# Kernel tuning notes

Measured on AMD Instinct MI355X. Metric: run time of the kernel, lower is better.

## Reference

```python
import jax, jax.numpy as jnp
import numpy as np

B = 4096          # fused tokens (batch)
E = 1024          # attnConfig embed_size == MoE emb_size
OUT = E // 4      # per-branch feature dim (self.output)
N_EXP = 8         # number of experts
TOP = 2           # top-k routing
H = 8             # attention heads
HD = E // H       # head dim
HID = 4 * E       # expert MLP hidden
IMG = 64 * 64     # flattened single-channel image
W_IMP = 0.01      # importance loss weight


def setup_inputs() -> dict:
    key = jax.random.key(0)
    ks = jax.random.split(key, 24)
    n = lambda i, shp, sc=1.0: jax.random.normal(ks[i], shp, jnp.float32) * sc
    inp = {
        'source': n(0, (B, 1, 64, 64)),
        'target': n(1, (B, 1, 64, 64)),
        'background': n(2, (B, 1, 64, 64)),
        'image': n(3, (B, E)),
        'text': n(4, (B, E)),
        # shared encoder (stub: flatten -> fc to OUT, shared across s/t/b)
        'W_enc': n(5, (IMG, OUT), 0.02), 'b_enc': jnp.zeros((OUT,), jnp.float32),
        # linerImg
        'W_img': n(6, (E, OUT), 0.02), 'b_img': jnp.zeros((OUT,), jnp.float32),
        # cross attention
        'Wq': n(7, (E, E), 0.02), 'bq': jnp.zeros((E,), jnp.float32),
        'Wk': n(8, (E, E), 0.02), 'bk': jnp.zeros((E,), jnp.float32),
        'Wv': n(9, (E, E), 0.02), 'bv': jnp.zeros((E,), jnp.float32),
        'Wo': n(10, (E, E), 0.02), 'bo': jnp.zeros((E,), jnp.float32),
        # gate
        'W_gate': n(11, (E, N_EXP), 0.02), 'b_gate': jnp.zeros((N_EXP,), jnp.float32),
        # experts: per-expert 2-layer MLP E->HID->E
        'W1': n(12, (N_EXP, E, HID), 0.02), 'b1': jnp.zeros((N_EXP, HID), jnp.float32),
        'W2': n(13, (N_EXP, HID, E), 0.02), 'b2': jnp.zeros((N_EXP, E), jnp.float32),
    }
    return inp


def reference(source, target, background, image, text,
              W_enc, b_enc, W_img, b_img,
              Wq, bq, Wk, bk, Wv, bv, Wo, bo,
              W_gate, b_gate, W1, b1, W2, b2):
    enc = lambda a: a.reshape(a.shape[0], -1) @ W_enc + b_enc      # shared_encoder stub
    s = enc(source); t = enc(target); bg = enc(background)        # [B, OUT] each
    img = jax.nn.silu(image @ W_img + b_img)                      # [B, OUT]
    x = jnp.concatenate([s, t, bg, img], axis=1)                  # [B, E] visionFeatures

    # cross attention with seq_len 1 for both x (query) and text (key/value)
    q = (x @ Wq + bq).reshape(B, H, HD)
    k = (text @ Wk + bk).reshape(B, H, HD)
    v = (text @ Wv + bv).reshape(B, H, HD)
    scores = jnp.sum(q * k, axis=-1, keepdims=True) / jnp.sqrt(jnp.float32(HD))  # [B,H,1]
    attw = jax.nn.softmax(scores[..., None], axis=-1)[..., 0]     # softmax over 1 key == 1
    att = (attw * v).reshape(B, E) @ Wo + bo                       # [B, E]

    gate_logits = att @ W_gate + b_gate                            # [B, N_EXP]
    gate_prob = jax.nn.softmax(gate_logits, axis=-1)               # eval mode: no noise
    top_w, top_idx = jax.lax.top_k(gate_prob, TOP)                 # [B, TOP]
    top_w = jax.nn.softmax(top_w, axis=-1)                         # renormalize over top-k

    # dense-dispatch equivalent of the per-expert gather/index_add loop
    h = jax.nn.gelu(jnp.einsum('be,neh->nbh', x, W1) + b1[:, None, :])   # [N,B,HID]
    y_all = jnp.einsum('nbh,nhe->nbe', h, W2) + b2[:, None, :]           # [N,B,E]
    combine = jnp.zeros((B, N_EXP), jnp.float32).at[
        jnp.arange(B)[:, None], top_idx].add(top_w)                      # [B,N]
    y = jnp.einsum('nbe,bn->be', y_all, combine)                          # [B,E]

    importance = gate_prob.sum(axis=0)                             # [N_EXP]
    importance_loss = W_IMP * (jnp.std(importance, ddof=1) / jnp.mean(importance)) ** 2
    return (y, gate_prob, importance_loss)
```

## Files before the change

### kernel.cpp

```cpp
#include <hip/hip_runtime.h>
#include <hip/hip_bf16.h>
#include <stdint.h>

typedef __bf16 bf16_t;
typedef bf16_t bf16x8 __attribute__((ext_vector_type(8)));
typedef float f32x4 __attribute__((ext_vector_type(4)));
typedef uint16_t u16x8 __attribute__((ext_vector_type(8)));

static constexpr int B_TOK  = 4096;
static constexpr int E_DIM  = 1024;
static constexpr int N_EXPC = 8;
static constexpr int HID    = 4096;
static constexpr int IMGSZ  = 4096;
static constexpr int NSLOT  = 2 * B_TOK;
static constexpr int NTIL   = 71;

#define DEVI __device__ __forceinline__

DEVI int imin(int a, int b) { return a < b ? a : b; }

DEVI uint16_t f2bf(float f) {
  union { float f; uint32_t u; } v; v.f = f;
  uint32_t u = v.u;
  return (uint16_t)((u + 0x7FFFu + ((u >> 16) & 1u)) >> 16);
}

DEVI void gload_lds16(const void* g, void* l) {
  __builtin_amdgcn_global_load_lds((const __attribute__((address_space(1))) void*)g,
                                   (__attribute__((address_space(3))) void*)l, 16, 0, 0);
}

template<int N> DEVI void waitv() {
  if constexpr (N == 0)       asm volatile("s_waitcnt vmcnt(0)" ::: "memory");
  else if constexpr (N == 3)  asm volatile("s_waitcnt vmcnt(3)" ::: "memory");
  else if constexpr (N == 4)  asm volatile("s_waitcnt vmcnt(4)" ::: "memory");
  else if constexpr (N == 10) asm volatile("s_waitcnt vmcnt(10)" ::: "memory");
}

#define BAR() do { __builtin_amdgcn_sched_barrier(0); __builtin_amdgcn_s_barrier(); \
                   __builtin_amdgcn_sched_barrier(0); } while (0)

#define MFMA16(a, b, c) __builtin_amdgcn_mfma_f32_16x16x32_bf16((a), (b), (c), 0, 0, 0)

__global__ __launch_bounds__(256)
void transW(const float* __restrict__ W1, const float* __restrict__ W2,
            const float* __restrict__ We, const float* __restrict__ Wi,
            uint16_t* __restrict__ W1T, uint16_t* __restrict__ W2T,
            uint16_t* __restrict__ WeT, uint16_t* __restrict__ WiT)
{
  __shared__ float tile[64][65];
  int bid = blockIdx.x;
  const float* in; uint16_t* out; int R, C, c0, r0;
  if (bid < 8192) {
    int e = bid >> 10, rem = bid & 1023;
    R = 1024; C = 4096;
    c0 = (rem & 63) * 64; r0 = (rem >> 6) * 64;
    in = W1 + (size_t)e * R * C; out = W1T + (size_t)e * R * C;
  } else if (bid < 16384) {
    int i = bid - 8192; int e = i >> 10, rem = i & 1023;
    R = 4096; C = 1024;
    c0 = (rem & 15) * 64; r0 = (rem >> 4) * 64;
    in = W2 + (size_t)e * R * C; out = W2T + (size_t)e * R * C;
  } else if (bid < 16640) {
    int i = bid - 16384;
    R = 4096; C = 256;
    c0 = (i & 3) * 64; r0 = (i >> 2) * 64;
    in = We; out = WeT;
  } else {
    int i = bid - 16640;
    R = 1024; C = 256;
    c0 = (i & 3) * 64; r0 = (i >> 2) * 64;
    in = Wi; out = WiT;
  }
  int t = threadIdx.x;
  #pragma unroll
  for (int i = 0; i < 4; ++i) {
    int rr = i * 16 + (t >> 4), c4 = (t & 15) * 4;
    f32x4 v = *(const f32x4*)&in[(size_t)(r0 + rr) * C + c0 + c4];
    tile[rr][c4 + 0] = v[0]; tile[rr][c4 + 1] = v[1];
    tile[rr][c4 + 2] = v[2]; tile[rr][c4 + 3] = v[3];
  }
  __syncthreads();
  #pragma unroll
  for (int i = 0; i < 2; ++i) {
    int c = i * 32 + (t >> 3), j = t & 7;
    u16x8 o;
    #pragma unroll
    for (int k = 0; k < 8; ++k) o[k] = f2bf(tile[j * 8 + k][c]);
    *(u16x8*)&out[(size_t)(c0 + c) * R + r0 + j * 8] = o;
  }
}

template<int BN, int EPI, bool GATHER, int NT, int KSPLIT>
__global__ __launch_bounds__(256, 5)
void gemm_p(const uint16_t* __restrict__ Ab, int lda,
            const uint16_t* __restrict__ BT, void* __restrict__ Cv, int ldc,
            const float* __restrict__ bias, int K,
            const int* __restrict__ meta, const int* __restrict__ perm,
            size_t bStride, int biasStride, size_t cPlane)
{
  constexpr int HN = BN / 2, FN = BN / 32;
  constexpr int OPS = (BN == 128 ? 4 : 3);
  constexpr int NT2 = NT * KSPLIT;
  constexpr int TOTAL = NTIL * NT2, Q = TOTAL / 8, FULLB = 64 * NT2;
  int bid = blockIdx.x;
  int wg = (bid & 7) * Q + (bid >> 3);
  int mtile, nt2;
  if (wg < FULLB) { int rem = wg % (8 * NT2); mtile = (wg / (8 * NT2)) * 8 + (rem & 7); nt2 = rem >> 3; }
  else            { int rem = wg - FULLB;     mtile = 64 + rem % 7;                     nt2 = rem / 7; }
  if (mtile >= meta[0]) return;
  int nt = nt2 % NT, kc = nt2 / NT;
  int e = meta[1 + 3 * mtile], rowBase = meta[2 + 3 * mtile], rows = meta[3 + 3 * mtile];
  int Kc = K / KSPLIT, k0 = kc * Kc;
  const uint16_t* Bt = BT + (size_t)e * bStride;
  const float* bi = bias + (size_t)e * (size_t)biasStride;

  constexpr int ABUF = 8192;
  constexpr int BBUF = (BN == 128) ? 8192 : 4096;
  __shared__ __align__(16) char sAraw[2 * ABUF];
  __shared__ __align__(16) char sBraw[2 * BBUF];

  int t = threadIdx.x, wave = t >> 6, lane = t & 63;
  int wr = wave >> 1, wc = wave & 1;

  int rB = t >> 2;
  int slB = ((t & 3) ^ (rB & 3)) * 8;
  const uint16_t* gB0 = Bt + (size_t)(nt * BN + rB) * K + k0 + slB;
  const uint16_t* gB1 = Bt + (size_t)(nt * BN + rB + 64) * K + k0 + slB;

  int r0 = t >> 2, r1 = r0 + 64;
  int sl = ((t & 3) ^ (r0 & 3)) * 8;
  int rr0 = imin(r0, rows - 1), rr1 = imin(r1, rows - 1);
  int car0 = GATHER ? perm[rowBase + rr0] : rowBase + rr0;
  int car1 = GATHER ? perm[rowBase + rr1] : rowBase + rr1;
  const uint16_t* gA0 = Ab + (size_t)car0 * lda + k0 + sl;
  const uint16_t* gA1 = Ab + (size_t)car1 * lda + k0 + sl;

  char* laW = sAraw + wave * 1024;
  char* lbW = sBraw + wave * 1024;
  auto STAGE = [&](int kt, int c) {
    int ko = kt << 5;
    char* la = laW + c * ABUF;
    char* lb = lbW + c * BBUF;
    gload_lds16(gA0 + ko, la);
    gload_lds16(gA1 + ko, la + 4096);
    gload_lds16(gB0 + ko, lb);
    if constexpr (BN == 128) gload_lds16(gB1 + ko, lb + 4096);
  };

  f32x4 acc[4][FN];
  #pragma unroll
  for (int m = 0; m < 4; m++)
    #pragma unroll
    for (int n = 0; n < FN; n++)
      acc[m][n] = f32x4{0.f, 0.f, 0.f, 0.f};

  STAGE(0, 0);

  int fr = lane & 15;
  int rdoff = ((lane >> 4) ^ (lane & 3)) * 16;
  int nk = Kc >> 5;

  for (int kt = 0; kt < nk; ++kt) {
    int b = kt & 1, nb = b ^ 1;
    bool more = kt + 1 < nk;
    if (more) { STAGE(kt + 1, nb); waitv<OPS>(); }
    else waitv<0>();
    BAR();

    const char* bA = sAraw + b * ABUF;
    const char* bB = sBraw + b * BBUF;
    bf16x8 af[4], bfr[FN];
    #pragma unroll
    for (int m = 0; m < 4; m++)
      af[m] = *(const bf16x8*)(bA + (wr * 64 + m * 16 + fr) * 64 + rdoff);
    #pragma unroll
    for (int n = 0; n < FN; n++)
      bfr[n] = *(const bf16x8*)(bB + (wc * HN + n * 16 + fr) * 64 + rdoff);
    #pragma unroll
    for (int m = 0; m < 4; m++)
      #pragma unroll
      for (int n = 0; n < FN; n++)
        acc[m][n] = MFMA16(af[m], bfr[n], acc[m][n]);

    BAR();
  }

  #pragma unroll
  for (int m = 0; m < 4; m++) {
    int lrow = wr * 64 + m * 16 + (lane >> 4) * 4;
    #pragma unroll
    for (int n = 0; n < FN; n++) {
      int col = nt * BN + wc * HN + n * 16 + (lane & 15);
      float bval = (EPI == 3) ? bi[col] : 0.f;
      #pragma unroll
      for (int r = 0; r < 4; r++) {
        int lr = lrow + r;
        if (lr >= rows) continue;
        float v = acc[m][n][r] + bval;
        size_t cr = (size_t)kc * cPlane + (size_t)(rowBase + lr) * ldc + col;
        if (EPI == 3) {
          float u = v + 0.044715f * v * v * v;
          v = v / (1.f + __expf(-1.5957691216057308f * u));
          ((uint16_t*)Cv)[cr] = f2bf(v);
        } else {
          ((float*)Cv)[cr] = v;
        }
      }
    }
  }
}

template<int SPLITK>
__global__ __launch_bounds__(256, 3)
void gemm_encR(const float* __restrict__ F0, const float* __restrict__ F1,
               const float* __restrict__ F2, int lda,
               const uint16_t* __restrict__ BT, float* __restrict__ P, int K)
{
  int z = blockIdx.z, br = z / SPLITK, kc = z % SPLITK;
  const float* Af = (br == 0) ? F0 : (br == 1) ? F1 : F2;
  int Kc = K / SPLITK, k0 = kc * Kc;
  int rowBase = blockIdx.x * 64, nt = blockIdx.y;

  __shared__ __align__(16) char sB[3 * 8192];
  int t = threadIdx.x, wave = t >> 6, lane = t & 63;
  int fr = lane & 15, q4 = lane >> 4;

  const float* gA = Af + (size_t)(rowBase + wave * 16 + fr) * lda + k0 + q4 * 8;

  int rloc = t >> 2;
  int ssw = ((t & 3) ^ (rloc & 3)) * 8;
  const uint16_t* gB0 = BT + (size_t)(nt * 128 + rloc) * K + k0 + ssw;
  const uint16_t* gB1 = gB0 + (size_t)64 * K;

  auto STB = [&](int kt, int c) {
    gload_lds16(gB0 + kt * 32, sB + c * 8192 + wave * 1024);
    gload_lds16(gB1 + kt * 32, sB + c * 8192 + 4096 + wave * 1024);
  };

  f32x4 acc[8];
  #pragma unroll
  for (int n = 0; n < 8; ++n) acc[n] = f32x4{0.f, 0.f, 0.f, 0.f};

  int nk = Kc >> 5;
  STB(0, 0); STB(1, 1);
  f32x4 aE0 = *(const f32x4*)(gA),      aE1 = *(const f32x4*)(gA + 4);
  f32x4 aO0 = *(const f32x4*)(gA + 32), aO1 = *(const f32x4*)(gA + 36);
  int c0 = 0, c2 = 2;
  int bRow = (q4 ^ (fr & 3)) * 16;

  auto step = [&](int kt, f32x4& aX0, f32x4& aX1) {
    bool m2 = kt + 2 < nk;
    if (m2) STB(kt + 2, c2);
    bf16x8 a;
    a[0] = (bf16_t)aX0[0]; a[1] = (bf16_t)aX0[1]; a[2] = (bf16_t)aX0[2]; a[3] = (bf16_t)aX0[3];
    a[4] = (bf16_t)aX1[0]; a[5] = (bf16_t)aX1[1]; a[6] = (bf16_t)aX1[2]; a[7] = (bf16_t)aX1[3];
    int kp = m2 ? kt + 2 : kt;
    aX0 = *(const f32x4*)(gA + kp * 32);
    aX1 = *(const f32x4*)(gA + kp * 32 + 4);
    if (m2) waitv<10>(); else waitv<0>();
    BAR();
    const char* bb = sB + c0 * 8192;
    bf16x8 bfr[8];
    #pragma unroll
    for (int n = 0; n < 8; ++n)
      bfr[n] = *(const bf16x8*)(bb + n * 1024 + fr * 64 + bRow);
    #pragma unroll
    for (int n = 0; n < 8; ++n) acc[n] = MFMA16(a, bfr[n], acc[n]);
    BAR();
    c0 = (c0 == 2) ? 0 : c0 + 1;
    c2 = (c2 == 2) ? 0 : c2 + 1;
  };

  for (int kt = 0; kt < nk; kt += 2) {
    step(kt, aE0, aE1);
    step(kt + 1, aO0, aO1);
  }

  #pragma unroll
  for (int n = 0; n < 8; ++n) {
    int col = nt * 128 + n * 16 + fr;
    #pragma unroll
    for (int r = 0; r < 4; ++r) {
      int row = rowBase + wave * 16 + q4 * 4 + r;
      P[((size_t)z * B_TOK + row) * 256 + col] = acc[n][r];
    }
  }
}

template<int SK, bool SILU>
__global__ __launch_bounds__(256)
void redu_k(const float* __restrict__ P, const float* __restrict__ bias,
            uint16_t* __restrict__ xb, int colBase)
{
  int br = blockIdx.y;
  int row = blockIdx.x * 4 + (threadIdx.x >> 6);
  int c4 = (threadIdx.x & 63) * 4;
  f32x4 s = *(const f32x4*)&bias[c4];
  const float* p = P + ((size_t)br * SK * B_TOK + row) * 256 + c4;
  #pragma unroll
  for (int kc = 0; kc < SK; ++kc)
    s += *(const f32x4*)(p + (size_t)kc * B_TOK * 256);
  if (SILU) {
    #pragma unroll
    for (int j = 0; j < 4; ++j) s[j] = s[j] / (1.f + __expf(-s[j]));
  }
  ushort4 o;
  o.x = f2bf(s[0]); o.y = f2bf(s[1]); o.z = f2bf(s[2]); o.w = f2bf(s[3]);
  *(ushort4*)&xb[(size_t)row * E_DIM + colBase + br * 256 + c4] = o;
}

__global__ __launch_bounds__(256)
void bvwo_k(const float* __restrict__ bv, const float* __restrict__ Wo,
            float* __restrict__ part)
{
  int b = blockIdx.x, t = threadIdx.x;
  f32x4 acc = {0.f, 0.f, 0.f, 0.f};
  for (int k = b * 128; k < b * 128 + 128; ++k) {
    float s = bv[k];
    f32x4 w = *(const f32x4*)&Wo[(size_t)k * E_DIM + t * 4];
    acc[0] = __builtin_fmaf(s, w[0], acc[0]);
    acc[1] = __builtin_fmaf(s, w[1], acc[1]);
    acc[2] = __builtin_fmaf(s, w[2], acc[2]);
    acc[3] = __builtin_fmaf(s, w[3], acc[3]);
  }
  *(f32x4*)&part[(size_t)b * E_DIM + t * 4] = acc;
}

__global__ void t1red_k(const float* __restrict__ part, const float* __restrict__ bo,
                        float* __restrict__ t1)
{
  int j = blockIdx.x * 256 + threadIdx.x;
  float s = bo[j];
  for (int b = 0; b < 8; ++b) s += part[(size_t)b * E_DIM + j];
  t1[j] = s;
}

__global__ __launch_bounds__(256)
void matf_k(const float* __restrict__ W, const float* __restrict__ G,
            float* __restrict__ out)
{
  int k = blockIdx.x * 4 + (threadIdx.x >> 6);
  int lane = threadIdx.x & 63;
  float a0 = 0.f, a1 = 0.f, a2 = 0.f, a3 = 0.f, a4 = 0.f, a5 = 0.f, a6 = 0.f, a7 = 0.f;
  for (int m = lane; m < E_DIM; m += 64) {
    float w = W[(size_t)k * E_DIM + m];
    const float* gm = &G[m * 8];
    a0 = __builtin_fmaf(w, gm[0], a0); a1 = __builtin_fmaf(w, gm[1], a1);
    a2 = __builtin_fmaf(w, gm[2], a2); a3 = __builtin_fmaf(w, gm[3], a3);
    a4 = __builtin_fmaf(w, gm[4], a4); a5 = __builtin_fmaf(w, gm[5], a5);
    a6 = __builtin_fmaf(w, gm[6], a6); a7 = __builtin_fmaf(w, gm[7], a7);
  }
  #pragma unroll
  for (int off = 32; off; off >>= 1) {
    a0 += __shfl_xor(a0, off); a1 += __shfl_xor(a1, off);
    a2 += __shfl_xor(a2, off); a3 += __shfl_xor(a3, off);
    a4 += __shfl_xor(a4, off); a5 += __shfl_xor(a5, off);
    a6 += __shfl_xor(a6, off); a7 += __shfl_xor(a7, off);
  }
  if (lane == 0) {
    float* o = &out[k * 8];
    o[0] = a0; o[1] = a1; o[2] = a2; o[3] = a3;
    o[4] = a4; o[5] = a5; o[6] = a6; o[7] = a7;
  }
}

__global__ __launch_bounds__(512)
void gbias_k(const float* __restrict__ t1, const float* __restrict__ Wg,
             const float* __restrict__ bg, float* __restrict__ gb)
{
  int e = threadIdx.x >> 6, lane = threadIdx.x & 63;
  float s = 0.f;
  for (int m = lane; m < E_DIM; m += 64) s = __builtin_fmaf(t1[m], Wg[m * 8 + e], s);
  #pragma unroll
  for (int off = 32; off; off >>= 1) s += __shfl_xor(s, off);
  if (lane == 0) gb[e] = s + bg[e];
}

__global__ __launch_bounds__(256)
void gate_k(const float* __restrict__ text, const float* __restrict__ G3,
            const float* __restrict__ gb, float* __restrict__ gate_out,
            int* __restrict__ topIdx, float* __restrict__ topW,
            int* __restrict__ counts)
{
  __shared__ __align__(16) float sT[E_DIM];
  __shared__ float lg[8];
  int b = blockIdx.x, t = threadIdx.x;
  *(f32x4*)&sT[t * 4] = *(const f32x4*)&text[(size_t)b * E_DIM + t * 4];
  __syncthreads();
  int wave = t >> 6, lane = t & 63;
  #pragma unroll
  for (int ei = 0; ei < 2; ++ei) {
    int e = wave * 2 + ei;
    float s = 0.f;
    for (int k = lane; k < E_DIM; k += 64) s = __builtin_fmaf(sT[k], G3[k * 8 + e], s);
    #pragma unroll
    for (int off = 32; off; off >>= 1) s += __shfl_down(s, off);
    if (lane == 0) lg[e] = s + gb[e];
  }
  __syncthreads();
  if (t == 0) {
    float p[8];
    float mx = lg[0];
    for (int i = 1; i < 8; i++) mx = fmaxf(mx, lg[i]);
    float den = 0.f;
    for (int i = 0; i < 8; i++) { p[i] = __expf(lg[i] - mx); den += p[i]; }
    float inv = 1.f / den;
    for (int i = 0; i < 8; i++) { p[i] *= inv; gate_out[(size_t)b * 8 + i] = p[i]; }
    int i1 = 0;
    for (int i = 1; i < 8; i++) if (p[i] > p[i1]) i1 = i;
    int i2 = (i1 == 0) ? 1 : 0;
    for (int i = 0; i < 8; i++) if (i != i1 && p[i] > p[i2]) i2 = i;
    float ex = __expf(p[i2] - p[i1]);
    float w1 = 1.f / (1.f + ex), w2 = ex / (1.f + ex);
    topIdx[b * 2] = i1; topIdx[b * 2 + 1] = i2;
    topW[b * 2] = w1;  topW[b * 2 + 1] = w2;
    atomicAdd(&counts[i1], 1);
    atomicAdd(&counts[i2], 1);
  }
}

__global__ void imp_k(const float* __restrict__ gate_out, float* __restrict__ imp)
{
  int e = blockIdx.x, t = threadIdx.x;
  float s = 0.f;
  for (int b = t; b < B_TOK; b += 256) s += gate_out[(size_t)b * 8 + e];
  __shared__ float red[256];
  red[t] = s; __syncthreads();
  for (int off = 128; off; off >>= 1) { if (t < off) red[t] += red[t + off]; __syncthreads(); }
  if (t == 0) imp[e] = red[0];
}

__global__ void loss_k(const float* __restrict__ imp, float* __restrict__ out_loss)
{
  if (threadIdx.x == 0 && blockIdx.x == 0) {
    float m = 0.f;
    for (int e = 0; e < 8; e++) m += imp[e];
    m *= 0.125f;
    float v = 0.f;
    for (int e = 0; e < 8; e++) { float d = imp[e] - m; v += d * d; }
    v /= 7.f;
    out_loss[0] = 0.01f * v / (m * m);
  }
}

__global__ void zero_k(int* counts, int* cursor)
{
  int t = threadIdx.x;
  if (t < 8) { counts[t] = 0; cursor[t] = 0; }
}

__global__ void scan_k(const int* __restrict__ counts, int* __restrict__ bases,
                       int* __restrict__ meta)
{
  if (threadIdx.x == 0) {
    int a = 0, nt = 0;
    for (int e = 0; e < 8; e++) {
      bases[e] = a;
      int c = counts[e];
      for (int j = 0; j < c; j += 128) {
        meta[1 + 3 * nt] = e;
        meta[2 + 3 * nt] = a + j;
        meta[3 + 3 * nt] = (c - j < 128) ? (c - j) : 128;
        nt++;
      }
      a += c;
    }
    meta[0] = nt;
  }
}

__global__ void fill_k(const int* __restrict__ topIdx, int* __restrict__ cursor,
                       const int* __restrict__ bases, int* __restrict__ perm,
                       int* __restrict__ slotOf)
{
  int b = blockIdx.x * 256 + threadIdx.x;
  if (b < B_TOK) {
    #pragma unroll
    for (int j = 0; j < 2; j++) {
      int e = topIdx[b * 2 + j];
      int pos = atomicAdd(&cursor[e], 1);
      int slot = bases[e] + pos;
      perm[slot] = b;
      slotOf[b * 2 + j] = slot;
    }
  }
}

__global__ __launch_bounds__(256)
void combine_k(const float* __restrict__ Yp, const int* __restrict__ slotOf,
               const int* __restrict__ topIdx, const float* __restrict__ topW,
               const float* __restrict__ b2, float* __restrict__ y)
{
  int b = blockIdx.x, t = threadIdx.x;
  int s0 = slotOf[b * 2], s1 = slotOf[b * 2 + 1];
  int e0 = topIdx[b * 2], e1 = topIdx[b * 2 + 1];
  float w0 = topW[b * 2], w1 = topW[b * 2 + 1];
  int c = t * 4;
  size_t P1 = (size_t)NSLOT * E_DIM;
  f32x4 x0 = *(const f32x4*)&Yp[(size_t)s0 * E_DIM + c];
  x0 += *(const f32x4*)&Yp[P1 + (size_t)s0 * E_DIM + c];
  x0 += *(const f32x4*)&b2[(size_t)e0 * E_DIM + c];
  f32x4 x1 = *(const f32x4*)&Yp[(size_t)s1 * E_DIM + c];
  x1 += *(const f32x4*)&Yp[P1 + (size_t)s1 * E_DIM + c];
  x1 += *(const f32x4*)&b2[(size_t)e1 * E_DIM + c];
  f32x4 r = x0 * w0 + x1 * w1;
  *(f32x4*)&y[(size_t)b * E_DIM + c] = r;
}

extern "C" void kernel_launch(void* const* d_in, const int* in_sizes, int n_in,
                              void* d_out, int out_size, void* d_ws, size_t ws_size,
                              hipStream_t stream)
{
  (void)in_sizes; (void)n_in; (void)out_size;
  const float* src   = (const float*)d_in[0];
  const float* tgt   = (const float*)d_in[1];
  const float* bgr   = (const float*)d_in[2];
  const float* image = (const float*)d_in[3];
  const float* text  = (const float*)d_in[4];
  const float* W_enc = (const float*)d_in[5];
  const float* b_enc = (const float*)d_in[6];
  const float* W_img = (const float*)d_in[7];
  const float* b_img = (const float*)d_in[8];
  const float* Wv    = (const float*)d_in[13];
  const float* bv    = (const float*)d_in[14];
  const float* Wo    = (const float*)d_in[15];
  const float* bo    = (const float*)d_in[16];
  const float* Wg    = (const float*)d_in[17];
  const float* bgg   = (const float*)d_in[18];
  const float* W1    = (const float*)d_in[19];
  const float* b1    = (const float*)d_in[20];
  const float* W2    = (const float*)d_in[21];
  const float* b2    = (const float*)d_in[22];

  float* out_y    = (float*)d_out;
  float* out_gate = out_y + (size_t)B_TOK * E_DIM;
  float* out_loss = out_gate + (size_t)B_TOK * N_EXPC;

  char* p = (char*)d_ws;
  auto alloc = [&](size_t bytes) { char* r = p; p += (bytes + 255) & ~(size_t)255; return r; };
  uint16_t* WencT = (uint16_t*)alloc((size_t)256 * IMGSZ * 2);
  uint16_t* WimgT = (uint16_t*)alloc((size_t)256 * E_DIM * 2);
  uint16_t* W1T   = (uint16_t*)alloc((size_t)N_EXPC * HID * E_DIM * 2);
  uint16_t* W2T   = (uint16_t*)alloc((size_t)N_EXPC * E_DIM * HID * 2);
  float* part  = (float*)alloc((size_t)8 * E_DIM * 4);
  float* g1c   = (float*)alloc((size_t)E_DIM * 8 * 4);
  float* G3    = (float*)alloc((size_t)E_DIM * 8 * 4);
  float* t1    = (float*)alloc(E_DIM * 4);
  float* gbv   = (float*)alloc(64 * 4);
  float* impb  = (float*)alloc(64 * 4);
  int*   topIdx = (int*)alloc(B_TOK * 2 * 4);
  float* topW   = (float*)alloc(B_TOK * 2 * 4);
  int*   slotOf = (int*)alloc(B_TOK * 2 * 4);
  int*   counts = (int*)alloc(64 * 4);
  int*   bases  = (int*)alloc(64 * 4);
  int*   cursor = (int*)alloc(64 * 4);
  int*   meta   = (int*)alloc((1 + 3 * (NTIL + 1)) * 4 + 64);
  int*   perm   = (int*)alloc(NSLOT * 4);
  uint16_t* xbf  = (uint16_t*)alloc((size_t)B_TOK * E_DIM * 2);
  uint16_t* Hbuf = (uint16_t*)alloc((size_t)NSLOT * HID * 2);
  char* uni = alloc((size_t)2 * NSLOT * E_DIM * 4);
  float* Penc = (float*)uni;
  float* Pimg = Penc + (size_t)12 * B_TOK * 256;
  float* Yp   = (float*)uni;
  if ((size_t)(p - (char*)d_ws) > ws_size) return;

  zero_k<<<1, 64, 0, stream>>>(counts, cursor);

  transW<<<dim3(16704), 256, 0, stream>>>(W1, W2, W_enc, W_img, W1T, W2T, WencT, WimgT);

  bvwo_k<<<8, 256, 0, stream>>>(bv, Wo, part);
  t1red_k<<<4, 256, 0, stream>>>(part, bo, t1);
  matf_k<<<256, 256, 0, stream>>>(Wo, Wg, g1c);
  matf_k<<<256, 256, 0, stream>>>(Wv, g1c, G3);
  gbias_k<<<1, 512, 0, stream>>>(t1, Wg, bgg, gbv);
  gate_k<<<B_TOK, 256, 0, stream>>>(text, G3, gbv, out_gate, topIdx, topW, counts);
  imp_k<<<8, 256, 0, stream>>>(out_gate, impb);
  loss_k<<<1, 64, 0, stream>>>(impb, out_loss);
  scan_k<<<1, 64, 0, stream>>>(counts, bases, meta);
  fill_k<<<16, 256, 0, stream>>>(topIdx, cursor, bases, perm, slotOf);

  gemm_encR<4><<<dim3(B_TOK / 64, 2, 12), 256, 0, stream>>>(
      src, tgt, bgr, IMGSZ, WencT, Penc, IMGSZ);
  gemm_encR<2><<<dim3(B_TOK / 64, 2, 2), 256, 0, stream>>>(
      image, image, image, E_DIM, WimgT, Pimg, E_DIM);
  redu_k<4, false><<<dim3(B_TOK / 4, 3), 256, 0, stream>>>(Penc, b_enc, xbf, 0);
  redu_k<2, true><<<dim3(B_TOK / 4, 1), 256, 0, stream>>>(Pimg, b_img, xbf, 768);

  gemm_p<128, 3, true, HID / 128, 1><<<dim3(NTIL * (HID / 128)), 256, 0, stream>>>(
      xbf, E_DIM, W1T, Hbuf, HID, b1, E_DIM, meta, perm, (size_t)HID * E_DIM, HID, 0);
  gemm_p<128, 0, false, E_DIM / 128, 2><<<dim3(NTIL * (E_DIM / 128) * 2), 256, 0, stream>>>(
      Hbuf, HID, W2T, Yp, E_DIM, b2, HID, meta, perm, (size_t)E_DIM * HID, E_DIM,
      (size_t)NSLOT * E_DIM);

  combine_k<<<B_TOK, 256, 0, stream>>>(Yp, slotOf, topIdx, topW, b2, out_y);
}
```

Before: 709.5 us.

## Fuse top-k combine into second expert GEMM epilogue via atomic scatter-add

The second expert GEMM now scales each output row by its routing weight and atomically adds it straight into the zeroed output, adding the bias in the epilogue. This removes the split-K partial buffer, the separate combine kernel and the large fp32 intermediate traffic. In exchange, split-K is dropped, which halves the number of workgroups, and float atomics add contention and make the summation order nondeterministic. Several small routing kernels are also merged (importance plus loss, scan plus fill using shared-memory cursors), and the output is zeroed with a memset.

```diff
diff --git a/kernel.cpp b/kernel.cpp
--- a/kernel.cpp
+++ b/kernel.cpp
@@ -97,6 +97,7 @@
             const uint16_t* __restrict__ BT, void* __restrict__ Cv, int ldc,
             const float* __restrict__ bias, int K,
             const int* __restrict__ meta, const int* __restrict__ perm,
+            const float* __restrict__ wSlot,
             size_t bStride, int biasStride, size_t cPlane)
 {
   constexpr int HN = BN / 2, FN = BN / 32;
@@ -186,25 +187,42 @@
     BAR();
   }
 
-  #pragma unroll
-  for (int m = 0; m < 4; m++) {
-    int lrow = wr * 64 + m * 16 + (lane >> 4) * 4;
-    #pragma unroll
-    for (int n = 0; n < FN; n++) {
-      int col = nt * BN + wc * HN + n * 16 + (lane & 15);
-      float bval = (EPI == 3) ? bi[col] : 0.f;
+  if constexpr (EPI == 4) {
+    float* outY = (float*)Cv;
+    #pragma unroll
+    for (int m = 0; m < 4; m++) {
       #pragma unroll
       for (int r = 0; r < 4; r++) {
-        int lr = lrow + r;
+        int lr = wr * 64 + m * 16 + (lane >> 4) * 4 + r;
         if (lr >= rows) continue;
-        float v = acc[m][n][r] + bval;
-        size_t cr = (size_t)kc * cPlane + (size_t)(rowBase + lr) * ldc + col;
-        if (EPI == 3) {
+        int slot = rowBase + lr;
+        int tok = perm[slot];
+        float w = wSlot[slot];
+        float* dst = outY + (size_t)tok * ldc;
+        #pragma unroll
+        for (int n = 0; n < FN; n++) {
+          int col = nt * BN + wc * HN + n * 16 + (lane & 15);
+          atomicAdd(dst + col, w * (acc[m][n][r] + bi[col]));
+        }
+      }
+    }
+  } else {
+    #pragma unroll
+    for (int m = 0; m < 4; m++) {
+      int lrow = wr * 64 + m * 16 + (lane >> 4) * 4;
+      #pragma unroll
+      for (int n = 0; n < FN; n++) {
+        int col = nt * BN + wc * HN + n * 16 + (lane & 15);
+        float bval = bi[col];
+        #pragma unroll
+        for (int r = 0; r < 4; r++) {
+          int lr = lrow + r;
+          if (lr >= rows) continue;
+          float v = acc[m][n][r] + bval;
+          size_t cr = (size_t)kc * cPlane + (size_t)(rowBase + lr) * ldc + col;
           float u = v + 0.044715f * v * v * v;
           v = v / (1.f + __expf(-1.5957691216057308f * u));
           ((uint16_t*)Cv)[cr] = f2bf(v);
-        } else {
-          ((float*)Cv)[cr] = v;
         }
       }
     }
@@ -420,43 +438,56 @@
   }
 }
 
-__global__ void imp_k(const float* __restrict__ gate_out, float* __restrict__ imp)
-{
-  int e = blockIdx.x, t = threadIdx.x;
-  float s = 0.f;
-  for (int b = t; b < B_TOK; b += 256) s += gate_out[(size_t)b * 8 + e];
-  __shared__ float red[256];
-  red[t] = s; __syncthreads();
-  for (int off = 128; off; off >>= 1) { if (t < off) red[t] += red[t + off]; __syncthreads(); }
-  if (t == 0) imp[e] = red[0];
-}
-
-__global__ void loss_k(const float* __restrict__ imp, float* __restrict__ out_loss)
-{
-  if (threadIdx.x == 0 && blockIdx.x == 0) {
+__global__ __launch_bounds__(256)
+void imploss_k(const float* __restrict__ gate_out, float* __restrict__ out_loss)
+{
+  int t = threadIdx.x;
+  float s[8] = {0.f, 0.f, 0.f, 0.f, 0.f, 0.f, 0.f, 0.f};
+  for (int b = t; b < B_TOK; b += 256) {
+    const float* g = &gate_out[(size_t)b * 8];
+    #pragma unroll
+    for (int e = 0; e < 8; ++e) s[e] += g[e];
+  }
+  __shared__ float red[8][256];
+  #pragma unroll
+  for (int e = 0; e < 8; ++e) red[e][t] = s[e];
+  __syncthreads();
+  for (int off = 128; off; off >>= 1) {
+    if (t < off)
+      #pragma unroll
+      for (int e = 0; e < 8; ++e) red[e][t] += red[e][t + off];
+    __syncthreads();
+  }
+  if (t == 0) {
     float m = 0.f;
-    for (int e = 0; e < 8; e++) m += imp[e];
+    for (int e = 0; e < 8; e++) m += red[e][0];
     m *= 0.125f;
     float v = 0.f;
-    for (int e = 0; e < 8; e++) { float d = imp[e] - m; v += d * d; }
+    for (int e = 0; e < 8; e++) { float d = red[e][0] - m; v += d * d; }
     v /= 7.f;
     out_loss[0] = 0.01f * v / (m * m);
   }
 }
 
-__global__ void zero_k(int* counts, int* cursor)
+__global__ void zero_k(int* counts)
 {
   int t = threadIdx.x;
-  if (t < 8) { counts[t] = 0; cursor[t] = 0; }
-}
-
-__global__ void scan_k(const int* __restrict__ counts, int* __restrict__ bases,
-                       int* __restrict__ meta)
-{
-  if (threadIdx.x == 0) {
+  if (t < 8) counts[t] = 0;
+}
+
+__global__ __launch_bounds__(256)
+void scanfill_k(const int* __restrict__ counts, const int* __restrict__ topIdx,
+                const float* __restrict__ topW,
+                int* __restrict__ meta, int* __restrict__ perm,
+                float* __restrict__ wSlot)
+{
+  __shared__ int sBases[8];
+  __shared__ int sCursor[8];
+  int t = threadIdx.x;
+  if (t == 0) {
     int a = 0, nt = 0;
     for (int e = 0; e < 8; e++) {
-      bases[e] = a;
+      sBases[e] = a; sCursor[e] = 0;
       int c = counts[e];
       for (int j = 0; j < c; j += 128) {
         meta[1 + 3 * nt] = e;
@@ -468,44 +499,17 @@
     }
     meta[0] = nt;
   }
-}
-
-__global__ void fill_k(const int* __restrict__ topIdx, int* __restrict__ cursor,
-                       const int* __restrict__ bases, int* __restrict__ perm,
-                       int* __restrict__ slotOf)
-{
-  int b = blockIdx.x * 256 + threadIdx.x;
-  if (b < B_TOK) {
+  __syncthreads();
+  for (int b = t; b < B_TOK; b += 256) {
     #pragma unroll
     for (int j = 0; j < 2; j++) {
       int e = topIdx[b * 2 + j];
-      int pos = atomicAdd(&cursor[e], 1);
-      int slot = bases[e] + pos;
+      int pos = atomicAdd(&sCursor[e], 1);
+      int slot = sBases[e] + pos;
       perm[slot] = b;
-      slotOf[b * 2 + j] = slot;
+      wSlot[slot] = topW[b * 2 + j];
     }
   }
-}
-
-__global__ __launch_bounds__(256)
-void combine_k(const float* __restrict__ Yp, const int* __restrict__ slotOf,
-               const int* __restrict__ topIdx, const float* __restrict__ topW,
-               const float* __restrict__ b2, float* __restrict__ y)
-{
-  int b = blockIdx.x, t = threadIdx.x;
-  int s0 = slotOf[b * 2], s1 = slotOf[b * 2 + 1];
-  int e0 = topIdx[b * 2], e1 = topIdx[b * 2 + 1];
-  float w0 = topW[b * 2], w1 = topW[b * 2 + 1];
-  int c = t * 4;
-  size_t P1 = (size_t)NSLOT * E_DIM;
-  f32x4 x0 = *(const f32x4*)&Yp[(size_t)s0 * E_DIM + c];
-  x0 += *(const f32x4*)&Yp[P1 + (size_t)s0 * E_DIM + c];
-  x0 += *(const f32x4*)&b2[(size_t)e0 * E_DIM + c];
-  f32x4 x1 = *(const f32x4*)&Yp[(size_t)s1 * E_DIM + c];
-  x1 += *(const f32x4*)&Yp[P1 + (size_t)s1 * E_DIM + c];
-  x1 += *(const f32x4*)&b2[(size_t)e1 * E_DIM + c];
-  f32x4 r = x0 * w0 + x1 * w1;
-  *(f32x4*)&y[(size_t)b * E_DIM + c] = r;
 }
 
 extern "C" void kernel_launch(void* const* d_in, const int* in_sizes, int n_in,
@@ -548,24 +552,21 @@
   float* G3    = (float*)alloc((size_t)E_DIM * 8 * 4);
   float* t1    = (float*)alloc(E_DIM * 4);
   float* gbv   = (float*)alloc(64 * 4);
-  float* impb  = (float*)alloc(64 * 4);
   int*   topIdx = (int*)alloc(B_TOK * 2 * 4);
   float* topW   = (float*)alloc(B_TOK * 2 * 4);
-  int*   slotOf = (int*)alloc(B_TOK * 2 * 4);
   int*   counts = (int*)alloc(64 * 4);
-  int*   bases  = (int*)alloc(64 * 4);
-  int*   cursor = (int*)alloc(64 * 4);
   int*   meta   = (int*)alloc((1 + 3 * (NTIL + 1)) * 4 + 64);
   int*   perm   = (int*)alloc(NSLOT * 4);
+  float* wSlot  = (float*)alloc(NSLOT * 4);
   uint16_t* xbf  = (uint16_t*)alloc((size_t)B_TOK * E_DIM * 2);
   uint16_t* Hbuf = (uint16_t*)alloc((size_t)NSLOT * HID * 2);
-  char* uni = alloc((size_t)2 * NSLOT * E_DIM * 4);
+  char* uni = alloc((size_t)14 * B_TOK * 256 * 4);
   float* Penc = (float*)uni;
   float* Pimg = Penc + (size_t)12 * B_TOK * 256;
-  float* Yp   = (float*)uni;
   if ((size_t)(p - (char*)d_ws) > ws_size) return;
 
-  zero_k<<<1, 64, 0, stream>>>(counts, cursor);
+  hipMemsetAsync(out_y, 0, (size_t)B_TOK * E_DIM * 4, stream);
+  zero_k<<<1, 64, 0, stream>>>(counts);
 
   transW<<<dim3(16704), 256, 0, stream>>>(W1, W2, W_enc, W_img, W1T, W2T, WencT, WimgT);
 
@@ -575,10 +576,8 @@
   matf_k<<<256, 256, 0, stream>>>(Wv, g1c, G3);
   gbias_k<<<1, 512, 0, stream>>>(t1, Wg, bgg, gbv);
   gate_k<<<B_TOK, 256, 0, stream>>>(text, G3, gbv, out_gate, topIdx, topW, counts);
-  imp_k<<<8, 256, 0, stream>>>(out_gate, impb);
-  loss_k<<<1, 64, 0, stream>>>(impb, out_loss);
-  scan_k<<<1, 64, 0, stream>>>(counts, bases, meta);
-  fill_k<<<16, 256, 0, stream>>>(topIdx, cursor, bases, perm, slotOf);
+  imploss_k<<<1, 256, 0, stream>>>(out_gate, out_loss);
+  scanfill_k<<<1, 256, 0, stream>>>(counts, topIdx, topW, meta, perm, wSlot);
 
   gemm_encR<4><<<dim3(B_TOK / 64, 2, 12), 256, 0, stream>>>(
       src, tgt, bgr, IMGSZ, WencT, Penc, IMGSZ);
@@ -588,10 +587,9 @@
   redu_k<2, true><<<dim3(B_TOK / 4, 1), 256, 0, stream>>>(Pimg, b_img, xbf, 768);
 
   gemm_p<128, 3, true, HID / 128, 1><<<dim3(NTIL * (HID / 128)), 256, 0, stream>>>(
-      xbf, E_DIM, W1T, Hbuf, HID, b1, E_DIM, meta, perm, (size_t)HID * E_DIM, HID, 0);
-  gemm_p<128, 0, false, E_DIM / 128, 2><<<dim3(NTIL * (E_DIM / 128) * 2), 256, 0, stream>>>(
-      Hbuf, HID, W2T, Yp, E_DIM, b2, HID, meta, perm, (size_t)E_DIM * HID, E_DIM,
-      (size_t)NSLOT * E_DIM);
-
-  combine_k<<<B_TOK, 256, 0, stream>>>(Yp, slotOf, topIdx, topW, b2, out_y);
-}
+      xbf, E_DIM, W1T, Hbuf, HID, b1, E_DIM, meta, perm, wSlot,
+      (size_t)HID * E_DIM, HID, 0);
+  gemm_p<128, 4, false, E_DIM / 128, 1><<<dim3(NTIL * (E_DIM / 128)), 256, 0, stream>>>(
+      Hbuf, HID, W2T, out_y, E_DIM, b2, HID, meta, perm, wSlot,
+      (size_t)E_DIM * HID, E_DIM, 0);
+}
```

After: 721.2 us. About the same (+1.6%).
